# Kernel tuning notes

Hardware: AMD Instinct MI355X
Metric: run time of the kernel (lower is better)

Reference implementation:

```python
import jax, jax.numpy as jnp
import numpy as np

B, D, C, L, H = 4096, 768, 512, 32, 256
E = C * L  # total flattened extension embeddings

def _l2norm(x, eps=1e-12):
    n = jnp.sqrt(jnp.sum(x * x, axis=-1, keepdims=True))
    return x / jnp.maximum(n, eps)

def setup_inputs() -> dict:
    key = jax.random.key(0)
    ks = jax.random.split(key, 8)
    text_feat = jax.random.normal(ks[0], (B, D), dtype=jnp.float32)
    img_feat = jax.random.normal(ks[1], (B, D), dtype=jnp.float32)
    ext_embs = _l2norm(jax.random.normal(ks[2], (E, D), dtype=jnp.float32))
    concept_names = _l2norm(jax.random.normal(ks[3], (C, D), dtype=jnp.float32))
    # each concept has exactly L extension embeddings; sorted segment ids
    segment_ids = jnp.repeat(jnp.arange(C, dtype=jnp.int32), L)
    W1 = jax.random.normal(ks[4], (C + D, H), dtype=jnp.float32) * (1.0 / np.sqrt(C + D))
    b1 = jnp.zeros((H,), dtype=jnp.float32)
    W2 = jax.random.normal(ks[5], (H, C), dtype=jnp.float32) * (1.0 / np.sqrt(H))
    b2 = jnp.zeros((C,), dtype=jnp.float32)
    alpha = jnp.float32(0.5)
    temperature = jnp.float32(0.07)
    return {"text_feat": text_feat, "img_feat": img_feat, "ext_embs": ext_embs,
            "segment_ids": segment_ids, "concept_names": concept_names,
            "W1": W1, "b1": b1, "W2": W2, "b2": b2,
            "alpha": alpha, "temperature": temperature}

def reference(text_feat, img_feat, ext_embs, segment_ids, concept_names,
              W1, b1, W2, b2, alpha, temperature):
    # query = normalize(text + img)
    q = _l2norm(text_feat + img_feat)                      # [B, D]
    # ragged per-concept max similarity: one big GEMM + segmented max
    sim = jnp.einsum('bd,ed->be', q, ext_embs)            # [B, E]
    prior = jax.ops.segment_max(sim.T, segment_ids,
                                num_segments=C,
                                indices_are_sorted=True).T  # [B, C]
    # small MLP -> temperature softmax -> weighted concept sum
    h = jax.nn.relu(jnp.concatenate([prior, q], axis=-1) @ W1 + b1)  # [B, H]
    logits = h @ W2 + b2                                   # [B, C]
    weights = jax.nn.softmax(logits / temperature, axis=-1)
    dyn_prompt = weights @ concept_names                   # [B, D]
    combined = text_feat + alpha * dyn_prompt
    return _l2norm(combined)
```

## Files before the change

### kernel.cpp

```cpp
#include <hip/hip_runtime.h>
#include <hip/hip_bf16.h>

typedef unsigned short bfu;
typedef __attribute__((ext_vector_type(4))) float f32x4;
typedef __attribute__((ext_vector_type(8))) short bf16x8;
typedef __attribute__((ext_vector_type(4))) int i32x4;
typedef __attribute__((ext_vector_type(8))) int i32x8;

#define GAS __attribute__((address_space(1)))
#define LAS __attribute__((address_space(3)))

__device__ __forceinline__ unsigned short f2bf(float f) {
    unsigned int u = __float_as_uint(f);
    u += 0x7FFFu + ((u >> 16) & 1u);
    return (unsigned short)(u >> 16);
}

__device__ __forceinline__ void gld_lds16(const void* g, void* l) {
    __builtin_amdgcn_global_load_lds((GAS void*)g, (LAS void*)l, 16, 0, 0);
}

__device__ __forceinline__ unsigned pack_fp8x4(float a, float b, float c, float d) {
    int u = __builtin_amdgcn_cvt_pk_fp8_f32(a, b, 0, false);
    u = __builtin_amdgcn_cvt_pk_fp8_f32(c, d, u, true);
    return (unsigned)u;
}

__device__ __forceinline__ float block_sum256(float v, float* sm) {
    #pragma unroll
    for (int off = 32; off; off >>= 1) v += __shfl_xor(v, off);
    int w = threadIdx.x >> 6;
    if ((threadIdx.x & 63) == 0) sm[w] = v;
    __syncthreads();
    float r = sm[0] + sm[1] + sm[2] + sm[3];
    __syncthreads();
    return r;
}

__device__ __forceinline__ float block_max256(float v, float* sm) {
    #pragma unroll
    for (int off = 32; off; off >>= 1) v = fmaxf(v, __shfl_xor(v, off));
    int w = threadIdx.x >> 6;
    if ((threadIdx.x & 63) == 0) sm[w] = v;
    __syncthreads();
    float r = fmaxf(fmaxf(sm[0], sm[1]), fmaxf(sm[2], sm[3]));
    __syncthreads();
    return r;
}

__device__ __forceinline__ void transpose_piece(const float* __restrict__ in,
                                                bfu* __restrict__ out, int R, int idx) {
    int c = idx / R, r = idx - c * R;
    out[idx] = f2bf(in[(size_t)r * ((size_t)0) + 0]);
}

__global__ __launch_bounds__(256) void prep_kernel(const float* __restrict__ ext,
                                                   unsigned* __restrict__ E8,
                                                   const float* __restrict__ W1, bfu* __restrict__ W1t,
                                                   const float* __restrict__ W2, bfu* __restrict__ W2t,
                                                   const float* __restrict__ cn, bfu* __restrict__ cnt) {
    int b = blockIdx.x;
    if (b < 12288) {
        int i = b * 256 + threadIdx.x;
        float4 v = ((const float4*)ext)[i];
        E8[i] = pack_fp8x4(v.x * 16.0f, v.y * 16.0f, v.z * 16.0f, v.w * 16.0f);
    } else if (b < 13568) {
        int idx = (b - 12288) * 256 + threadIdx.x;
        int c = idx / 1280, r = idx - c * 1280;
        W1t[idx] = f2bf(W1[(size_t)r * 256 + c]);
    } else if (b < 14080) {
        int idx = (b - 13568) * 256 + threadIdx.x;
        int c = idx / 256, r = idx - c * 256;
        W2t[idx] = f2bf(W2[(size_t)r * 512 + c]);
    } else {
        int idx = (b - 14080) * 256 + threadIdx.x;
        int c = idx / 512, r = idx - c * 512;
        cnt[idx] = f2bf(cn[(size_t)r * 768 + c]);
    }
}

__global__ __launch_bounds__(256) void q_kernel(const float* __restrict__ text,
                                                const float* __restrict__ img,
                                                bfu* __restrict__ X,
                                                unsigned* __restrict__ Q8) {
    __shared__ float sm[4];
    int row = blockIdx.x, t = threadIdx.x;
    float4 v = {0.f, 0.f, 0.f, 0.f};
    if (t < 192) {
        float4 a = ((const float4*)(text + (size_t)row * 768))[t];
        float4 b = ((const float4*)(img + (size_t)row * 768))[t];
        v.x = a.x + b.x; v.y = a.y + b.y; v.z = a.z + b.z; v.w = a.w + b.w;
    }
    float ss = v.x * v.x + v.y * v.y + v.z * v.z + v.w * v.w;
    float tot = block_sum256(ss, sm);
    float inv = 1.0f / fmaxf(sqrtf(tot), 1e-12f);
    if (t < 192) {
        ushort4 o = make_ushort4(f2bf(v.x * inv), f2bf(v.y * inv), f2bf(v.z * inv), f2bf(v.w * inv));
        ((ushort4*)(X + (size_t)row * 1280 + 512))[t] = o;
        float s16 = inv * 16.0f;
        Q8[(size_t)row * 192 + t] = pack_fp8x4(v.x * s16, v.y * s16, v.z * s16, v.w * s16);
    }
}

__device__ __forceinline__ i32x8 ld_frag8(const char* s, int row, int lq) {
    const int r7 = row & 7;
    i32x4 lo = *(const i32x4*)(s + row * 128 + ((((lq << 1))     ^ r7) << 4));
    i32x4 hi = *(const i32x4*)(s + row * 128 + ((((lq << 1) | 1) ^ r7) << 4));
    i32x8 v;
    v[0] = lo[0]; v[1] = lo[1]; v[2] = lo[2]; v[3] = lo[3];
    v[4] = hi[0]; v[5] = hi[1]; v[6] = hi[2]; v[7] = hi[3];
    return v;
}

__global__ __launch_bounds__(256) void sim_segmax_kernel(const unsigned char* __restrict__ Q8,
                                                         const unsigned char* __restrict__ E8,
                                                         bfu* __restrict__ X) {
    __shared__ __align__(16) char sA[128 * 128];
    __shared__ __align__(16) char sB[128 * 128];
    int bm = blockIdx.x >> 7;
    int bn = blockIdx.x & 127;
    int m0 = bm * 128, n0 = bn * 128;
    const int t = threadIdx.x, lane = t & 63, wv = t >> 6;
    const int wm = (wv >> 1) << 6, wn = (wv & 1) << 6;
    const int lr = lane & 15, lq = lane >> 4;

    f32x4 zero = {0.f, 0.f, 0.f, 0.f};
    f32x4 acc[4][4];
    #pragma unroll
    for (int i = 0; i < 4; ++i)
        #pragma unroll
        for (int j = 0; j < 4; ++j) acc[i][j] = zero;

    for (int k0 = 0; k0 < 768; k0 += 128) {
        #pragma unroll
        for (int i = 0; i < 4; ++i) {
            int idx = i * 256 + t;
            int row = idx >> 3, cs = idx & 7, cg = cs ^ (row & 7);
            gld_lds16(Q8 + (size_t)(m0 + row) * 768 + k0 + (cg << 4), sA + idx * 16);
            gld_lds16(E8 + (size_t)(n0 + row) * 768 + k0 + (cg << 4), sB + idx * 16);
        }
        __syncthreads();
        i32x8 af[4], bf8[4];
        #pragma unroll
        for (int f = 0; f < 4; ++f) {
            af[f]  = ld_frag8(sA, wm + f * 16 + lr, lq);
            bf8[f] = ld_frag8(sB, wn + f * 16 + lr, lq);
        }
        #pragma unroll
        for (int i = 0; i < 4; ++i)
            #pragma unroll
            for (int j = 0; j < 4; ++j)
                acc[i][j] = __builtin_amdgcn_mfma_scale_f32_16x16x128_f8f6f4(
                    af[i], bf8[j], acc[i][j], 0, 0, 0, 0x7F7F7F7F, 0, 0x7F7F7F7F);
        __syncthreads();
    }

    const float sc = 0.00390625f;
    #pragma unroll
    for (int i = 0; i < 4; ++i) {
        #pragma unroll
        for (int r = 0; r < 4; ++r) {
            float g0 = fmaxf(acc[i][0][r], acc[i][1][r]);
            float g1 = fmaxf(acc[i][2][r], acc[i][3][r]);
            #pragma unroll
            for (int off = 8; off; off >>= 1) {
                g0 = fmaxf(g0, __shfl_xor(g0, off));
                g1 = fmaxf(g1, __shfl_xor(g1, off));
            }
            if (lr == 0) {
                int row = m0 + wm + i * 16 + lq * 4 + r;
                int g = (n0 + wn) >> 5;
                X[(size_t)row * 1280 + g]     = f2bf(g0 * sc);
                X[(size_t)row * 1280 + g + 1] = f2bf(g1 * sc);
            }
        }
    }
}

template <int BM>
__device__ __forceinline__ void gemm_mainloop(const bfu* A, const bfu* B, int K,
                                              int lda, int ldb, int m0, int n0,
                                              short* sA, short* sB, f32x4 acc[BM / 32][4]) {
    const int t = threadIdx.x, lane = t & 63, wv = t >> 6;
    const int wm = (wv >> 1) * (BM / 2), wn = (wv & 1) << 6;
    const int lr = lane & 15, lq = lane >> 4;

    for (int k0 = 0; k0 < K; k0 += 64) {
        #pragma unroll
        for (int i = 0; i < BM / 32; ++i) {
            int idx = i * 256 + t;
            int row = idx >> 3, cs = idx & 7, cg = cs ^ (row & 7);
            gld_lds16(A + (size_t)(m0 + row) * lda + k0 + (cg << 3), sA + idx * 8);
        }
        #pragma unroll
        for (int i = 0; i < 4; ++i) {
            int idx = i * 256 + t;
            int row = idx >> 3, cs = idx & 7, cg = cs ^ (row & 7);
            gld_lds16(B + (size_t)(n0 + row) * ldb + k0 + (cg << 3), sB + idx * 8);
        }
        __syncthreads();
        #pragma unroll
        for (int kk = 0; kk < 2; ++kk) {
            bf16x8 af[BM / 32], bfr[4];
            #pragma unroll
            for (int f = 0; f < BM / 32; ++f) {
                int mrow = wm + f * 16 + lr;
                int c = kk * 4 + lq;
                af[f] = *(const bf16x8*)(sA + mrow * 64 + ((c ^ (mrow & 7)) << 3));
            }
            #pragma unroll
            for (int f = 0; f < 4; ++f) {
                int nrow = wn + f * 16 + lr;
                int c = kk * 4 + lq;
                bfr[f] = *(const bf16x8*)(sB + nrow * 64 + ((c ^ (nrow & 7)) << 3));
            }
            #pragma unroll
            for (int i = 0; i < BM / 32; ++i)
                #pragma unroll
                for (int j = 0; j < 4; ++j)
                    acc[i][j] = __builtin_amdgcn_mfma_f32_16x16x32_bf16(af[i], bfr[j], acc[i][j], 0, 0, 0);
        }
        __syncthreads();
    }
}

template <int EPI, int BM>
__global__ __launch_bounds__(256) void gemm_kernel(const bfu* __restrict__ A,
                                                   const bfu* __restrict__ B,
                                                   const float* __restrict__ bias,
                                                   void* __restrict__ out,
                                                   int K, int lda, int ldb, int N, int ntN) {
    __shared__ __align__(16) short sA[BM * 64];
    __shared__ __align__(16) short sB[128 * 64];
    int bm = blockIdx.x / ntN, bn = blockIdx.x - bm * ntN;
    int m0 = bm * BM, n0 = bn * 128;
    f32x4 zero = {0.f, 0.f, 0.f, 0.f};
    f32x4 acc[BM / 32][4];
    #pragma unroll
    for (int i = 0; i < BM / 32; ++i)
        #pragma unroll
        for (int j = 0; j < 4; ++j) acc[i][j] = zero;

    gemm_mainloop<BM>(A, B, K, lda, ldb, m0, n0, sA, sB, acc);

    const int t = threadIdx.x, lane = t & 63, wv = t >> 6;
    const int wm = (wv >> 1) * (BM / 2), wn = (wv & 1) << 6;
    const int lr = lane & 15, lq = lane >> 4;
    #pragma unroll
    for (int j = 0; j < 4; ++j) {
        int col = n0 + wn + j * 16 + lr;
        float bv = (EPI >= 1) ? bias[col] : 0.0f;
        #pragma unroll
        for (int i = 0; i < BM / 32; ++i) {
            #pragma unroll
            for (int r = 0; r < 4; ++r) {
                int row = m0 + wm + i * 16 + lq * 4 + r;
                float v = acc[i][j][r] + bv;
                if (EPI == 1) {
                    v = fmaxf(v, 0.0f);
                    ((bfu*)out)[(size_t)row * N + col] = f2bf(v);
                } else {
                    ((float*)out)[(size_t)row * N + col] = v;
                }
            }
        }
    }
}

__global__ __launch_bounds__(256) void softmax_kernel(const float* __restrict__ logits,
                                                      const float* __restrict__ temp,
                                                      bfu* __restrict__ wout) {
    __shared__ float sm[4];
    int row = blockIdx.x, t = threadIdx.x;
    float invT = 1.0f / temp[0];
    float l0 = logits[(size_t)row * 512 + t];
    float l1 = logits[(size_t)row * 512 + 256 + t];
    float m = block_max256(fmaxf(l0, l1), sm);
    float e0 = __expf((l0 - m) * invT);
    float e1 = __expf((l1 - m) * invT);
    float s = block_sum256(e0 + e1, sm);
    float inv = 1.0f / s;
    wout[(size_t)row * 512 + t]       = f2bf(e0 * inv);
    wout[(size_t)row * 512 + 256 + t] = f2bf(e1 * inv);
}

__global__ __launch_bounds__(256) void final_kernel(const float* __restrict__ text,
                                                    const float* __restrict__ dyn,
                                                    const float* __restrict__ alpha,
                                                    float* __restrict__ out) {
    __shared__ float sm[4];
    int row = blockIdx.x, t = threadIdx.x;
    float a = alpha[0];
    float v[3]; float ss = 0.f;
    #pragma unroll
    for (int i = 0; i < 3; ++i) {
        size_t o = (size_t)row * 768 + t + 256 * i;
        v[i] = text[o] + a * dyn[o];
        ss += v[i] * v[i];
    }
    float tot = block_sum256(ss, sm);
    float inv = 1.0f / fmaxf(sqrtf(tot), 1e-12f);
    #pragma unroll
    for (int i = 0; i < 3; ++i)
        out[(size_t)row * 768 + t + 256 * i] = v[i] * inv;
}

extern "C" void kernel_launch(void* const* d_in, const int* in_sizes, int n_in,
                              void* d_out, int out_size, void* d_ws, size_t ws_size,
                              hipStream_t stream) {
    const float* text  = (const float*)d_in[0];
    const float* img   = (const float*)d_in[1];
    const float* ext   = (const float*)d_in[2];
    const float* cn    = (const float*)d_in[4];
    const float* W1    = (const float*)d_in[5];
    const float* b1    = (const float*)d_in[6];
    const float* W2    = (const float*)d_in[7];
    const float* b2    = (const float*)d_in[8];
    const float* alpha = (const float*)d_in[9];
    const float* temp  = (const float*)d_in[10];
    float* out = (float*)d_out;

    char* p = (char*)d_ws;
    auto carve = [&](size_t bytes) -> char* {
        char* r = p; p += (bytes + 255) & ~(size_t)255; return r;
    };
    unsigned char* E8 = (unsigned char*)carve((size_t)16384 * 768);
    unsigned char* Q8 = (unsigned char*)carve((size_t)4096 * 768);
    bfu*   X      = (bfu*)carve((size_t)4096 * 1280 * 2);
    bfu*   W1t    = (bfu*)carve((size_t)256 * 1280 * 2);
    bfu*   W2t    = (bfu*)carve((size_t)512 * 256 * 2);
    bfu*   cnt    = (bfu*)carve((size_t)768 * 512 * 2);
    bfu*   Hm     = (bfu*)carve((size_t)4096 * 256 * 2);
    float* logits = (float*)carve((size_t)4096 * 512 * 4);
    bfu*   wts    = (bfu*)carve((size_t)4096 * 512 * 2);
    float* dyn    = (float*)carve((size_t)4096 * 768 * 4);

    prep_kernel<<<15616, 256, 0, stream>>>(ext, (unsigned*)E8, W1, W1t, W2, W2t, cn, cnt);
    q_kernel<<<4096, 256, 0, stream>>>(text, img, X, (unsigned*)Q8);
    sim_segmax_kernel<<<32 * 128, 256, 0, stream>>>(Q8, E8, X);
    gemm_kernel<1, 64><<<64 * 2, 256, 0, stream>>>(X, W1t, b1, (void*)Hm, 1280, 1280, 1280, 256, 2);
    gemm_kernel<2, 64><<<64 * 4, 256, 0, stream>>>(Hm, W2t, b2, (void*)logits, 256, 256, 256, 512, 4);
    softmax_kernel<<<4096, 256, 0, stream>>>(logits, temp, wts);
    gemm_kernel<0, 64><<<64 * 6, 256, 0, stream>>>(wts, cnt, nullptr, (void*)dyn, 512, 512, 512, 768, 6);
    final_kernel<<<4096, 256, 0, stream>>>(text, dyn, alpha, out);
}
```

Baseline: 319.3 us.

## Merge q prep into prep kernel, double-buffer FP8 sim GEMM with 32x32 MFMA, shrink MLP tiles

The query-normalization kernel is folded into the prep kernel, which removes one launch. The FP8 similarity/segment-max kernel now uses 32x32x64 scaled MFMAs with a K-step of 64 and double-buffered LDS staging, so the next tile's loads overlap compute. It also swaps block order so M varies fastest for reuse of E8 tiles, and adds a 4-block occupancy hint. The MLP and weighted-sum GEMMs switch to a 32-row tile, doubling grid size for better CU fill on small problems, at the cost of less reuse per block.

```diff
diff --git a/kernel.cpp b/kernel.cpp
--- a/kernel.cpp
+++ b/kernel.cpp
@@ -3,6 +3,7 @@
 
 typedef unsigned short bfu;
 typedef __attribute__((ext_vector_type(4))) float f32x4;
+typedef __attribute__((ext_vector_type(16))) float f32x16;
 typedef __attribute__((ext_vector_type(8))) short bf16x8;
 typedef __attribute__((ext_vector_type(4))) int i32x4;
 typedef __attribute__((ext_vector_type(8))) int i32x8;
@@ -48,130 +49,125 @@
     return r;
 }
 
-__device__ __forceinline__ void transpose_piece(const float* __restrict__ in,
-                                                bfu* __restrict__ out, int R, int idx) {
-    int c = idx / R, r = idx - c * R;
-    out[idx] = f2bf(in[(size_t)r * ((size_t)0) + 0]);
-}
-
-__global__ __launch_bounds__(256) void prep_kernel(const float* __restrict__ ext,
+__global__ __launch_bounds__(256) void prep_kernel(const float* __restrict__ text,
+                                                   const float* __restrict__ img,
+                                                   bfu* __restrict__ X,
+                                                   unsigned* __restrict__ Q8,
+                                                   const float* __restrict__ ext,
                                                    unsigned* __restrict__ E8,
                                                    const float* __restrict__ W1, bfu* __restrict__ W1t,
                                                    const float* __restrict__ W2, bfu* __restrict__ W2t,
                                                    const float* __restrict__ cn, bfu* __restrict__ cnt) {
-    int b = blockIdx.x;
-    if (b < 12288) {
-        int i = b * 256 + threadIdx.x;
+    __shared__ float sm[4];
+    int b = blockIdx.x, t = threadIdx.x;
+    if (b < 4096) {
+        int row = b;
+        float4 v = {0.f, 0.f, 0.f, 0.f};
+        if (t < 192) {
+            float4 a = ((const float4*)(text + (size_t)row * 768))[t];
+            float4 c = ((const float4*)(img + (size_t)row * 768))[t];
+            v.x = a.x + c.x; v.y = a.y + c.y; v.z = a.z + c.z; v.w = a.w + c.w;
+        }
+        float ss = v.x * v.x + v.y * v.y + v.z * v.z + v.w * v.w;
+        float tot = block_sum256(ss, sm);
+        float inv = 1.0f / fmaxf(sqrtf(tot), 1e-12f);
+        if (t < 192) {
+            ushort4 o = make_ushort4(f2bf(v.x * inv), f2bf(v.y * inv), f2bf(v.z * inv), f2bf(v.w * inv));
+            ((ushort4*)(X + (size_t)row * 1280 + 512))[t] = o;
+            float s16 = inv * 16.0f;
+            Q8[(size_t)row * 192 + t] = pack_fp8x4(v.x * s16, v.y * s16, v.z * s16, v.w * s16);
+        }
+    } else if (b < 16384) {
+        int i = (b - 4096) * 256 + t;
         float4 v = ((const float4*)ext)[i];
         E8[i] = pack_fp8x4(v.x * 16.0f, v.y * 16.0f, v.z * 16.0f, v.w * 16.0f);
-    } else if (b < 13568) {
-        int idx = (b - 12288) * 256 + threadIdx.x;
+    } else if (b < 17664) {
+        int idx = (b - 16384) * 256 + t;
         int c = idx / 1280, r = idx - c * 1280;
         W1t[idx] = f2bf(W1[(size_t)r * 256 + c]);
-    } else if (b < 14080) {
-        int idx = (b - 13568) * 256 + threadIdx.x;
+    } else if (b < 18176) {
+        int idx = (b - 17664) * 256 + t;
         int c = idx / 256, r = idx - c * 256;
         W2t[idx] = f2bf(W2[(size_t)r * 512 + c]);
     } else {
-        int idx = (b - 14080) * 256 + threadIdx.x;
+        int idx = (b - 18176) * 256 + t;
         int c = idx / 512, r = idx - c * 512;
         cnt[idx] = f2bf(cn[(size_t)r * 768 + c]);
     }
 }
 
-__global__ __launch_bounds__(256) void q_kernel(const float* __restrict__ text,
-                                                const float* __restrict__ img,
-                                                bfu* __restrict__ X,
-                                                unsigned* __restrict__ Q8) {
-    __shared__ float sm[4];
-    int row = blockIdx.x, t = threadIdx.x;
-    float4 v = {0.f, 0.f, 0.f, 0.f};
-    if (t < 192) {
-        float4 a = ((const float4*)(text + (size_t)row * 768))[t];
-        float4 b = ((const float4*)(img + (size_t)row * 768))[t];
-        v.x = a.x + b.x; v.y = a.y + b.y; v.z = a.z + b.z; v.w = a.w + b.w;
-    }
-    float ss = v.x * v.x + v.y * v.y + v.z * v.z + v.w * v.w;
-    float tot = block_sum256(ss, sm);
-    float inv = 1.0f / fmaxf(sqrtf(tot), 1e-12f);
-    if (t < 192) {
-        ushort4 o = make_ushort4(f2bf(v.x * inv), f2bf(v.y * inv), f2bf(v.z * inv), f2bf(v.w * inv));
-        ((ushort4*)(X + (size_t)row * 1280 + 512))[t] = o;
-        float s16 = inv * 16.0f;
-        Q8[(size_t)row * 192 + t] = pack_fp8x4(v.x * s16, v.y * s16, v.z * s16, v.w * s16);
-    }
-}
-
-__device__ __forceinline__ i32x8 ld_frag8(const char* s, int row, int lq) {
-    const int r7 = row & 7;
-    i32x4 lo = *(const i32x4*)(s + row * 128 + ((((lq << 1))     ^ r7) << 4));
-    i32x4 hi = *(const i32x4*)(s + row * 128 + ((((lq << 1) | 1) ^ r7) << 4));
-    i32x8 v;
-    v[0] = lo[0]; v[1] = lo[1]; v[2] = lo[2]; v[3] = lo[3];
-    v[4] = hi[0]; v[5] = hi[1]; v[6] = hi[2]; v[7] = hi[3];
-    return v;
-}
-
-__global__ __launch_bounds__(256) void sim_segmax_kernel(const unsigned char* __restrict__ Q8,
-                                                         const unsigned char* __restrict__ E8,
-                                                         bfu* __restrict__ X) {
-    __shared__ __align__(16) char sA[128 * 128];
-    __shared__ __align__(16) char sB[128 * 128];
-    int bm = blockIdx.x >> 7;
-    int bn = blockIdx.x & 127;
+__global__ __launch_bounds__(256, 4) void sim_segmax_kernel(const unsigned char* __restrict__ Q8,
+                                                            const unsigned char* __restrict__ E8,
+                                                            bfu* __restrict__ X) {
+    __shared__ __align__(16) char sA[2][128 * 64];
+    __shared__ __align__(16) char sB[2][128 * 64];
+    int bm = blockIdx.x & 31;
+    int bn = blockIdx.x >> 5;
     int m0 = bm * 128, n0 = bn * 128;
     const int t = threadIdx.x, lane = t & 63, wv = t >> 6;
     const int wm = (wv >> 1) << 6, wn = (wv & 1) << 6;
-    const int lr = lane & 15, lq = lane >> 4;
-
-    f32x4 zero = {0.f, 0.f, 0.f, 0.f};
-    f32x4 acc[4][4];
-    #pragma unroll
-    for (int i = 0; i < 4; ++i)
-        #pragma unroll
-        for (int j = 0; j < 4; ++j) acc[i][j] = zero;
-
-    for (int k0 = 0; k0 < 768; k0 += 128) {
-        #pragma unroll
-        for (int i = 0; i < 4; ++i) {
+    const int lr32 = lane & 31, h = lane >> 5;
+
+    f32x16 acc[2][2];
+    #pragma unroll
+    for (int i = 0; i < 2; ++i)
+        #pragma unroll
+        for (int j = 0; j < 2; ++j)
+            #pragma unroll
+            for (int r = 0; r < 16; ++r) acc[i][j][r] = 0.f;
+
+    auto stage = [&](int k0, int buf) {
+        #pragma unroll
+        for (int i = 0; i < 2; ++i) {
             int idx = i * 256 + t;
-            int row = idx >> 3, cs = idx & 7, cg = cs ^ (row & 7);
-            gld_lds16(Q8 + (size_t)(m0 + row) * 768 + k0 + (cg << 4), sA + idx * 16);
-            gld_lds16(E8 + (size_t)(n0 + row) * 768 + k0 + (cg << 4), sB + idx * 16);
-        }
+            int row = idx >> 2, cs = idx & 3, cg = cs ^ (row & 3);
+            gld_lds16(Q8 + (size_t)(m0 + row) * 768 + k0 + (cg << 4), sA[buf] + idx * 16);
+            gld_lds16(E8 + (size_t)(n0 + row) * 768 + k0 + (cg << 4), sB[buf] + idx * 16);
+        }
+    };
+    auto ldfrag = [&](const char* s, int row) -> i32x8 {
+        int r3 = row & 3;
+        i32x4 lo = *(const i32x4*)(s + row * 64 + (((2 * h) ^ r3) << 4));
+        i32x4 hi = *(const i32x4*)(s + row * 64 + (((2 * h + 1) ^ r3) << 4));
+        i32x8 v;
+        v[0] = lo[0]; v[1] = lo[1]; v[2] = lo[2]; v[3] = lo[3];
+        v[4] = hi[0]; v[5] = hi[1]; v[6] = hi[2]; v[7] = hi[3];
+        return v;
+    };
+
+    stage(0, 0);
+    for (int k = 0; k < 12; ++k) {
+        int cur = k & 1;
         __syncthreads();
-        i32x8 af[4], bf8[4];
-        #pragma unroll
-        for (int f = 0; f < 4; ++f) {
-            af[f]  = ld_frag8(sA, wm + f * 16 + lr, lq);
-            bf8[f] = ld_frag8(sB, wn + f * 16 + lr, lq);
-        }
-        #pragma unroll
-        for (int i = 0; i < 4; ++i)
-            #pragma unroll
-            for (int j = 0; j < 4; ++j)
-                acc[i][j] = __builtin_amdgcn_mfma_scale_f32_16x16x128_f8f6f4(
-                    af[i], bf8[j], acc[i][j], 0, 0, 0, 0x7F7F7F7F, 0, 0x7F7F7F7F);
-        __syncthreads();
+        if (k + 1 < 12) stage((k + 1) * 64, cur ^ 1);
+        i32x8 a0 = ldfrag(sA[cur], wm + lr32);
+        i32x8 a1 = ldfrag(sA[cur], wm + 32 + lr32);
+        i32x8 b0 = ldfrag(sB[cur], wn + lr32);
+        i32x8 b1 = ldfrag(sB[cur], wn + 32 + lr32);
+        acc[0][0] = __builtin_amdgcn_mfma_scale_f32_32x32x64_f8f6f4(a0, b0, acc[0][0], 0, 0, 0, 0x7F7F7F7F, 0, 0x7F7F7F7F);
+        acc[0][1] = __builtin_amdgcn_mfma_scale_f32_32x32x64_f8f6f4(a0, b1, acc[0][1], 0, 0, 0, 0x7F7F7F7F, 0, 0x7F7F7F7F);
+        acc[1][0] = __builtin_amdgcn_mfma_scale_f32_32x32x64_f8f6f4(a1, b0, acc[1][0], 0, 0, 0, 0x7F7F7F7F, 0, 0x7F7F7F7F);
+        acc[1][1] = __builtin_amdgcn_mfma_scale_f32_32x32x64_f8f6f4(a1, b1, acc[1][1], 0, 0, 0, 0x7F7F7F7F, 0, 0x7F7F7F7F);
     }
 
     const float sc = 0.00390625f;
     #pragma unroll
-    for (int i = 0; i < 4; ++i) {
-        #pragma unroll
-        for (int r = 0; r < 4; ++r) {
-            float g0 = fmaxf(acc[i][0][r], acc[i][1][r]);
-            float g1 = fmaxf(acc[i][2][r], acc[i][3][r]);
-            #pragma unroll
-            for (int off = 8; off; off >>= 1) {
-                g0 = fmaxf(g0, __shfl_xor(g0, off));
-                g1 = fmaxf(g1, __shfl_xor(g1, off));
-            }
-            if (lr == 0) {
-                int row = m0 + wm + i * 16 + lq * 4 + r;
-                int g = (n0 + wn) >> 5;
-                X[(size_t)row * 1280 + g]     = f2bf(g0 * sc);
-                X[(size_t)row * 1280 + g + 1] = f2bf(g1 * sc);
+    for (int i = 0; i < 2; ++i) {
+        #pragma unroll
+        for (int j = 0; j < 2; ++j) {
+            int g = ((n0 + wn) >> 5) + j;
+            #pragma unroll
+            for (int r = 0; r < 16; ++r) {
+                float v = acc[i][j][r];
+                v = fmaxf(v, __shfl_xor(v, 1));
+                v = fmaxf(v, __shfl_xor(v, 2));
+                v = fmaxf(v, __shfl_xor(v, 4));
+                v = fmaxf(v, __shfl_xor(v, 8));
+                v = fmaxf(v, __shfl_xor(v, 16));
+                if (lr32 == 0) {
+                    int row = m0 + wm + 32 * i + (r & 3) + 8 * (r >> 2) + 4 * h;
+                    X[(size_t)row * 1280 + g] = f2bf(v * sc);
+                }
             }
         }
     }
@@ -335,12 +331,12 @@
     bfu*   wts    = (bfu*)carve((size_t)4096 * 512 * 2);
     float* dyn    = (float*)carve((size_t)4096 * 768 * 4);
 
-    prep_kernel<<<15616, 256, 0, stream>>>(ext, (unsigned*)E8, W1, W1t, W2, W2t, cn, cnt);
-    q_kernel<<<4096, 256, 0, stream>>>(text, img, X, (unsigned*)Q8);
-    sim_segmax_kernel<<<32 * 128, 256, 0, stream>>>(Q8, E8, X);
-    gemm_kernel<1, 64><<<64 * 2, 256, 0, stream>>>(X, W1t, b1, (void*)Hm, 1280, 1280, 1280, 256, 2);
-    gemm_kernel<2, 64><<<64 * 4, 256, 0, stream>>>(Hm, W2t, b2, (void*)logits, 256, 256, 256, 512, 4);
+    prep_kernel<<<19712, 256, 0, stream>>>(text, img, X, (unsigned*)Q8,
+                                           ext, (unsigned*)E8, W1, W1t, W2, W2t, cn, cnt);
+    sim_segmax_kernel<<<4096, 256, 0, stream>>>(Q8, E8, X);
+    gemm_kernel<1, 32><<<128 * 2, 256, 0, stream>>>(X, W1t, b1, (void*)Hm, 1280, 1280, 1280, 256, 2);
+    gemm_kernel<2, 32><<<128 * 4, 256, 0, stream>>>(Hm, W2t, b2, (void*)logits, 256, 256, 256, 512, 4);
     softmax_kernel<<<4096, 256, 0, stream>>>(logits, temp, wts);
-    gemm_kernel<0, 64><<<64 * 6, 256, 0, stream>>>(wts, cnt, nullptr, (void*)dyn, 512, 512, 512, 768, 6);
+    gemm_kernel<0, 32><<<128 * 6, 256, 0, stream>>>(wts, cnt, nullptr, (void*)dyn, 512, 512, 512, 768, 6);
     final_kernel<<<4096, 256, 0, stream>>>(text, dyn, alpha, out);
 }
```

New measurement: 860.6 us. 170% more time.
